# Performance work log

Hardware: AMD Instinct MI355X
Metric: run time of the kernel (lower is better)

The kernel has to match this reference:

```python
import jax, jax.numpy as jnp
import numpy as np

NUM_TOKENS = 50265  # roberta-base vocab size
CONTEXT_LEN = 384
BS = 4
N_DATASET = 2048


def setup_inputs() -> dict:
    key = jax.random.key(0)
    k1, k2, k3 = jax.random.split(key, 3)
    dataset_tokens = jax.random.randint(k1, (N_DATASET, CONTEXT_LEN), 0, NUM_TOKENS)
    input_tokens = jax.random.randint(k2, (BS, CONTEXT_LEN), 0, NUM_TOKENS)
    # t in (0,1): avoid exact endpoints where log((1-t)/T) -> -inf
    t = jax.random.uniform(k3, (BS,), minval=0.05, maxval=0.95, dtype=jnp.float32)
    return {"input_tokens": input_tokens, "dataset_tokens": dataset_tokens, "t": t}


def reference(input_tokens, dataset_tokens, t):
    """EmpiricalDFM.calculate_uniform_probabilities, dataset given as one array.

    flow[b,c,s] = sum_n exp(logp[n,b]) * onehot(dataset_tokens)[n,c,s] / sum_n exp(logp[n,b])
               = sum_n softmax_n(logp[:,b]) * onehot(dataset_tokens)[n,c,s]
    The original torch code computes exactly this via an online (streamed)
    log-sum-exp accumulation over dataset batches; softmax over the full
    dataset axis is the mathematically identical single-pass form.
    """
    bs, c = input_tokens.shape
    n = dataset_tokens.shape[0]
    T = NUM_TOKENS

    # (n, bs): number of positions where dataset row matches input row
    match_count = (dataset_tokens[:, None, :] == input_tokens[None, :, :]).sum(-1).astype(t.dtype)

    log_a = jnp.log(t + (1.0 - t) / T)          # (bs,) prob of match per position
    log_b = jnp.log((1.0 - t) / T)              # (bs,) prob of mismatch per position
    logp = match_count * log_a[None, :] + (c - match_count) * log_b[None, :]  # (n, bs)

    # Normalized weights over the dataset axis (stable log-sum-exp built in).
    w = jax.nn.softmax(logp, axis=0)            # (n, bs)

    # Weighted one-hot accumulate WITHOUT materializing the (n,c,V) one-hot:
    # flow[b, pos, dataset_tokens[j, pos]] += w[j, b]
    c_idx = jnp.broadcast_to(jnp.arange(c)[None, :], (n, c))
    flow = jnp.zeros((bs, c, T), dtype=t.dtype)
    flow = flow.at[:, c_idx, dataset_tokens].add(w.T[:, :, None])  # scatter over (bs, n, c)
    return flow
```

## Files before the change

kernel.cpp:

```cpp
#include <hip/hip_runtime.h>

constexpr int T_VOCAB = 50265;
constexpr int CLEN    = 384;
constexpr int BSZ     = 4;
constexpr int NDATA   = 2048;
constexpr int NPT     = NDATA / 256;
constexpr int CHUNK   = 12672;

template <bool WRITE_T>
__global__ __launch_bounds__(256) void k_match_logp(
    const int* __restrict__ in_tok,
    const int* __restrict__ ds_tok,
    const float* __restrict__ t,
    float* __restrict__ logp,
    int* __restrict__ dsT)
{
    __shared__ int s_in[BSZ * CLEN];
    __shared__ float s_la[BSZ], s_lb[BSZ];
    const int tid = threadIdx.x;
    for (int i = tid; i < BSZ * CLEN; i += 256) s_in[i] = in_tok[i];
    if (tid < BSZ) {
        float tv = t[tid];
        s_la[tid] = logf(tv + (1.0f - tv) / (float)T_VOCAB);
        s_lb[tid] = logf((1.0f - tv) / (float)T_VOCAB);
    }
    __syncthreads();

    const int n = blockIdx.x * 256 + tid;
    int mc0 = 0, mc1 = 0, mc2 = 0, mc3 = 0;
    const int4* row = (const int4*)(ds_tok + (size_t)n * CLEN);
    #pragma unroll 8
    for (int j = 0; j < CLEN / 4; ++j) {
        int4 v = row[j];
        int s = 4 * j;
        if (WRITE_T) {
            dsT[(size_t)(s + 0) * NDATA + n] = v.x;
            dsT[(size_t)(s + 1) * NDATA + n] = v.y;
            dsT[(size_t)(s + 2) * NDATA + n] = v.z;
            dsT[(size_t)(s + 3) * NDATA + n] = v.w;
        }
        mc0 += (v.x == s_in[0*CLEN+s]) + (v.y == s_in[0*CLEN+s+1]) + (v.z == s_in[0*CLEN+s+2]) + (v.w == s_in[0*CLEN+s+3]);
        mc1 += (v.x == s_in[1*CLEN+s]) + (v.y == s_in[1*CLEN+s+1]) + (v.z == s_in[1*CLEN+s+2]) + (v.w == s_in[1*CLEN+s+3]);
        mc2 += (v.x == s_in[2*CLEN+s]) + (v.y == s_in[2*CLEN+s+1]) + (v.z == s_in[2*CLEN+s+2]) + (v.w == s_in[2*CLEN+s+3]);
        mc3 += (v.x == s_in[3*CLEN+s]) + (v.y == s_in[3*CLEN+s+1]) + (v.z == s_in[3*CLEN+s+2]) + (v.w == s_in[3*CLEN+s+3]);
    }
    float m;
    m = (float)mc0; logp[0 * NDATA + n] = m * s_la[0] + ((float)CLEN - m) * s_lb[0];
    m = (float)mc1; logp[1 * NDATA + n] = m * s_la[1] + ((float)CLEN - m) * s_lb[1];
    m = (float)mc2; logp[2 * NDATA + n] = m * s_la[2] + ((float)CLEN - m) * s_lb[2];
    m = (float)mc3; logp[3 * NDATA + n] = m * s_la[3] + ((float)CLEN - m) * s_lb[3];
}

__global__ __launch_bounds__(256) void k_softmax(
    const float* __restrict__ logp,
    float* __restrict__ w)
{
    const int b = blockIdx.x;
    const int tid = threadIdx.x;
    float lp[NPT];
    float m = -INFINITY;
    #pragma unroll
    for (int k = 0; k < NPT; ++k) {
        lp[k] = logp[b * NDATA + tid + k * 256];
        m = fmaxf(m, lp[k]);
    }
    #pragma unroll
    for (int off = 32; off >= 1; off >>= 1) m = fmaxf(m, __shfl_xor(m, off));
    __shared__ float redm[4];
    __shared__ float reds[4];
    const int wid = tid >> 6;
    if ((tid & 63) == 0) redm[wid] = m;
    __syncthreads();
    const float M = fmaxf(fmaxf(redm[0], redm[1]), fmaxf(redm[2], redm[3]));

    float e[NPT];
    float sum = 0.0f;
    #pragma unroll
    for (int k = 0; k < NPT; ++k) { e[k] = expf(lp[k] - M); sum += e[k]; }
    #pragma unroll
    for (int off = 32; off >= 1; off >>= 1) sum += __shfl_xor(sum, off);
    if ((tid & 63) == 0) reds[wid] = sum;
    __syncthreads();
    const float inv = 1.0f / (reds[0] + reds[1] + reds[2] + reds[3]);
    #pragma unroll
    for (int k = 0; k < NPT; ++k) w[b * NDATA + tid + k * 256] = e[k] * inv;
}

template <bool USE_T>
__global__ __launch_bounds__(256) void k_scatter(
    const int* __restrict__ ds_tok,
    const int* __restrict__ dsT,
    const float* __restrict__ w,
    float* __restrict__ out)
{
    __shared__ float lds[CHUNK];
    const int tid = threadIdx.x;
    const int bid = blockIdx.x;
    const int b = bid & (BSZ - 1);
    const int s = bid >> 2;

    int   tok[NPT];
    float wv[NPT];
    #pragma unroll
    for (int k = 0; k < NPT; ++k) {
        const int n = tid + k * 256;
        tok[k] = USE_T ? dsT[(size_t)s * NDATA + n]
                       : ds_tok[(size_t)n * CLEN + s];
        wv[k] = w[b * NDATA + n];
    }

    float* rowp = out + ((size_t)b * CLEN + s) * T_VOCAB;
    const size_t row_elem0 = ((size_t)b * CLEN + s) * (size_t)T_VOCAB;

    for (int c0 = 0; c0 < T_VOCAB; c0 += CHUNK) {
        const int nch = (T_VOCAB - c0 < CHUNK) ? (T_VOCAB - c0) : CHUNK;
        for (int i = tid; i < nch; i += 256) lds[i] = 0.0f;
        __syncthreads();
        #pragma unroll
        for (int k = 0; k < NPT; ++k) {
            const unsigned off = (unsigned)(tok[k] - c0);
            if (off < (unsigned)nch) atomicAdd(&lds[off], wv[k]);
        }
        __syncthreads();
        const unsigned g0mod = (unsigned)((row_elem0 + (size_t)c0) & 3u);
        int head = (int)((4u - g0mod) & 3u);
        if (head > nch) head = nch;
        if (tid < head) rowp[c0 + tid] = lds[tid];
        const int rem = nch - head;
        const int nv = rem >> 2;
        float4* dst4 = (float4*)(rowp + c0 + head);
        for (int i = tid; i < nv; i += 256) {
            const int j = head + 4 * i;
            float4 v = { lds[j], lds[j + 1], lds[j + 2], lds[j + 3] };
            dst4[i] = v;
        }
        const int ts = head + (nv << 2);
        for (int i = ts + tid; i < nch; i += 256) rowp[c0 + i] = lds[i];
        __syncthreads();
    }
}

extern "C" void kernel_launch(void* const* d_in, const int* in_sizes, int n_in,
                              void* d_out, int out_size, void* d_ws, size_t ws_size,
                              hipStream_t stream) {
    const int*   in_tok = (const int*)d_in[0];
    const int*   ds_tok = (const int*)d_in[1];
    const float* t      = (const float*)d_in[2];
    float* out = (float*)d_out;

    float* logp = (float*)d_ws;
    float* w    = logp + (size_t)BSZ * NDATA;
    int*   dsT  = (int*)(w + (size_t)BSZ * NDATA);

    const size_t need = (size_t)2 * BSZ * NDATA * sizeof(float)
                      + (size_t)CLEN * NDATA * sizeof(int);
    const bool use_t = ws_size >= need;

    if (use_t) {
        k_match_logp<true><<<NDATA / 256, 256, 0, stream>>>(in_tok, ds_tok, t, logp, dsT);
    } else {
        k_match_logp<false><<<NDATA / 256, 256, 0, stream>>>(in_tok, ds_tok, t, logp, dsT);
    }
    k_softmax<<<BSZ, 256, 0, stream>>>(logp, w);
    if (use_t) {
        k_scatter<true><<<BSZ * CLEN, 256, 0, stream>>>(ds_tok, dsT, w, out);
    } else {
        k_scatter<false><<<BSZ * CLEN, 256, 0, stream>>>(ds_tok, dsT, w, out);
    }
}
```

Measured before the change: 351.9 us.

## Split match into tiled transpose plus sliced counting; fuse weights; nontemporal scatter stores

Replaces the single 8-block match kernel, which also wrote an uncoalesced transpose, with a shared-memory tiled transpose kernel and a 64-block sliced match-count kernel writing partial counts. A new weights kernel sums the partial counts, computes logp and does the softmax. The scatter kernel gets a smaller LDS chunk so more blocks fit per CU, an aligned LDS offset so it can copy whole vectors, and nontemporal vector stores for the large output. This adds two kernel launches and a partial-count buffer in exchange for more parallelism in the early stages and cheaper output writes.

```diff
diff --git a/kernel.cpp b/kernel.cpp
--- a/kernel.cpp
+++ b/kernel.cpp
@@ -5,69 +5,85 @@
 constexpr int BSZ     = 4;
 constexpr int NDATA   = 2048;
 constexpr int NPT     = NDATA / 256;
-constexpr int CHUNK   = 12672;
-
-template <bool WRITE_T>
-__global__ __launch_bounds__(256) void k_match_logp(
+constexpr int CHUNK   = 6720;
+constexpr int SLICES  = 8;
+constexpr int SCOLS   = CLEN / SLICES;
+
+typedef float f32x4 __attribute__((ext_vector_type(4)));
+
+__global__ __launch_bounds__(256) void k_transpose(
+    const int* __restrict__ ds, int* __restrict__ dsT)
+{
+    __shared__ int tile[64][65];
+    const int n0 = blockIdx.x * 64;
+    const int s0 = blockIdx.y * 64;
+    const int lane = threadIdx.x & 63;
+    const int quad = threadIdx.x >> 6;
+    #pragma unroll
+    for (int k = 0; k < 16; ++k) {
+        const int r = quad + 4 * k;
+        tile[r][lane] = ds[(size_t)(n0 + r) * CLEN + s0 + lane];
+    }
+    __syncthreads();
+    #pragma unroll
+    for (int k = 0; k < 16; ++k) {
+        const int c = quad + 4 * k;
+        dsT[(size_t)(s0 + c) * NDATA + n0 + lane] = tile[lane][c];
+    }
+}
+
+__global__ __launch_bounds__(256) void k_match(
+    const int* __restrict__ dsT,
     const int* __restrict__ in_tok,
-    const int* __restrict__ ds_tok,
+    int* __restrict__ pcount)
+{
+    const int nt = blockIdx.x & 7;
+    const int sl = blockIdx.x >> 3;
+    const int n  = nt * 256 + threadIdx.x;
+    const int sbase = sl * SCOLS;
+    int c0 = 0, c1 = 0, c2 = 0, c3 = 0;
+    #pragma unroll 4
+    for (int j = 0; j < SCOLS; ++j) {
+        const int s = sbase + j;
+        const int tok = dsT[(size_t)s * NDATA + n];
+        c0 += (tok == in_tok[0 * CLEN + s]);
+        c1 += (tok == in_tok[1 * CLEN + s]);
+        c2 += (tok == in_tok[2 * CLEN + s]);
+        c3 += (tok == in_tok[3 * CLEN + s]);
+    }
+    pcount[(sl * BSZ + 0) * NDATA + n] = c0;
+    pcount[(sl * BSZ + 1) * NDATA + n] = c1;
+    pcount[(sl * BSZ + 2) * NDATA + n] = c2;
+    pcount[(sl * BSZ + 3) * NDATA + n] = c3;
+}
+
+__global__ __launch_bounds__(256) void k_weights(
+    const int* __restrict__ pcount,
     const float* __restrict__ t,
-    float* __restrict__ logp,
-    int* __restrict__ dsT)
-{
-    __shared__ int s_in[BSZ * CLEN];
-    __shared__ float s_la[BSZ], s_lb[BSZ];
-    const int tid = threadIdx.x;
-    for (int i = tid; i < BSZ * CLEN; i += 256) s_in[i] = in_tok[i];
-    if (tid < BSZ) {
-        float tv = t[tid];
-        s_la[tid] = logf(tv + (1.0f - tv) / (float)T_VOCAB);
-        s_lb[tid] = logf((1.0f - tv) / (float)T_VOCAB);
-    }
-    __syncthreads();
-
-    const int n = blockIdx.x * 256 + tid;
-    int mc0 = 0, mc1 = 0, mc2 = 0, mc3 = 0;
-    const int4* row = (const int4*)(ds_tok + (size_t)n * CLEN);
-    #pragma unroll 8
-    for (int j = 0; j < CLEN / 4; ++j) {
-        int4 v = row[j];
-        int s = 4 * j;
-        if (WRITE_T) {
-            dsT[(size_t)(s + 0) * NDATA + n] = v.x;
-            dsT[(size_t)(s + 1) * NDATA + n] = v.y;
-            dsT[(size_t)(s + 2) * NDATA + n] = v.z;
-            dsT[(size_t)(s + 3) * NDATA + n] = v.w;
-        }
-        mc0 += (v.x == s_in[0*CLEN+s]) + (v.y == s_in[0*CLEN+s+1]) + (v.z == s_in[0*CLEN+s+2]) + (v.w == s_in[0*CLEN+s+3]);
-        mc1 += (v.x == s_in[1*CLEN+s]) + (v.y == s_in[1*CLEN+s+1]) + (v.z == s_in[1*CLEN+s+2]) + (v.w == s_in[1*CLEN+s+3]);
-        mc2 += (v.x == s_in[2*CLEN+s]) + (v.y == s_in[2*CLEN+s+1]) + (v.z == s_in[2*CLEN+s+2]) + (v.w == s_in[2*CLEN+s+3]);
-        mc3 += (v.x == s_in[3*CLEN+s]) + (v.y == s_in[3*CLEN+s+1]) + (v.z == s_in[3*CLEN+s+2]) + (v.w == s_in[3*CLEN+s+3]);
-    }
-    float m;
-    m = (float)mc0; logp[0 * NDATA + n] = m * s_la[0] + ((float)CLEN - m) * s_lb[0];
-    m = (float)mc1; logp[1 * NDATA + n] = m * s_la[1] + ((float)CLEN - m) * s_lb[1];
-    m = (float)mc2; logp[2 * NDATA + n] = m * s_la[2] + ((float)CLEN - m) * s_lb[2];
-    m = (float)mc3; logp[3 * NDATA + n] = m * s_la[3] + ((float)CLEN - m) * s_lb[3];
-}
-
-__global__ __launch_bounds__(256) void k_softmax(
-    const float* __restrict__ logp,
     float* __restrict__ w)
 {
     const int b = blockIdx.x;
     const int tid = threadIdx.x;
+    const float tv = t[b];
+    const float la = logf(tv + (1.0f - tv) / (float)T_VOCAB);
+    const float lb = logf((1.0f - tv) / (float)T_VOCAB);
+
     float lp[NPT];
     float m = -INFINITY;
     #pragma unroll
     for (int k = 0; k < NPT; ++k) {
-        lp[k] = logp[b * NDATA + tid + k * 256];
+        const int n = tid + k * 256;
+        int cnt = 0;
+        #pragma unroll
+        for (int sl = 0; sl < SLICES; ++sl)
+            cnt += pcount[(sl * BSZ + b) * NDATA + n];
+        const float mc = (float)cnt;
+        lp[k] = mc * la + ((float)CLEN - mc) * lb;
         m = fmaxf(m, lp[k]);
     }
     #pragma unroll
     for (int off = 32; off >= 1; off >>= 1) m = fmaxf(m, __shfl_xor(m, off));
-    __shared__ float redm[4];
-    __shared__ float reds[4];
+    __shared__ float redm[4], reds[4];
     const int wid = tid >> 6;
     if ((tid & 63) == 0) redm[wid] = m;
     __syncthreads();
@@ -93,7 +109,7 @@
     const float* __restrict__ w,
     float* __restrict__ out)
 {
-    __shared__ float lds[CHUNK];
+    __shared__ float lds[CHUNK + 4];
     const int tid = threadIdx.x;
     const int bid = blockIdx.x;
     const int b = bid & (BSZ - 1);
@@ -109,35 +125,99 @@
         wv[k] = w[b * NDATA + n];
     }
 
-    float* rowp = out + ((size_t)b * CLEN + s) * T_VOCAB;
     const size_t row_elem0 = ((size_t)b * CLEN + s) * (size_t)T_VOCAB;
+    float* rowp = out + row_elem0;
+    const int align_off = (int)(row_elem0 & 3);
 
     for (int c0 = 0; c0 < T_VOCAB; c0 += CHUNK) {
         const int nch = (T_VOCAB - c0 < CHUNK) ? (T_VOCAB - c0) : CHUNK;
-        for (int i = tid; i < nch; i += 256) lds[i] = 0.0f;
+        const int tot = nch + align_off;
+        f32x4* l4 = (f32x4*)lds;
+        const int nz4 = (tot + 3) >> 2;
+        for (int i = tid; i < nz4; i += 256) l4[i] = (f32x4){0.f, 0.f, 0.f, 0.f};
         __syncthreads();
         #pragma unroll
         for (int k = 0; k < NPT; ++k) {
             const unsigned off = (unsigned)(tok[k] - c0);
-            if (off < (unsigned)nch) atomicAdd(&lds[off], wv[k]);
+            if (off < (unsigned)nch) atomicAdd(&lds[off + align_off], wv[k]);
         }
         __syncthreads();
-        const unsigned g0mod = (unsigned)((row_elem0 + (size_t)c0) & 3u);
-        int head = (int)((4u - g0mod) & 3u);
+        int head = (4 - align_off) & 3;
         if (head > nch) head = nch;
-        if (tid < head) rowp[c0 + tid] = lds[tid];
-        const int rem = nch - head;
-        const int nv = rem >> 2;
-        float4* dst4 = (float4*)(rowp + c0 + head);
-        for (int i = tid; i < nv; i += 256) {
-            const int j = head + 4 * i;
-            float4 v = { lds[j], lds[j + 1], lds[j + 2], lds[j + 3] };
-            dst4[i] = v;
-        }
+        if (tid < head) rowp[c0 + tid] = lds[tid + align_off];
+        const int nv = (nch - head) >> 2;
+        const f32x4* l4s = (const f32x4*)lds + (align_off ? 1 : 0);
+        f32x4* dst4 = (f32x4*)(rowp + c0 + head);
+        for (int i = tid; i < nv; i += 256)
+            __builtin_nontemporal_store(l4s[i], &dst4[i]);
         const int ts = head + (nv << 2);
-        for (int i = ts + tid; i < nch; i += 256) rowp[c0 + i] = lds[i];
+        for (int i = ts + tid; i < nch; i += 256) rowp[c0 + i] = lds[i + align_off];
         __syncthreads();
     }
+}
+
+__global__ __launch_bounds__(256) void k_match_logp_fb(
+    const int* __restrict__ in_tok, const int* __restrict__ ds_tok,
+    const float* __restrict__ t, float* __restrict__ logp)
+{
+    __shared__ int s_in[BSZ * CLEN];
+    __shared__ float s_la[BSZ], s_lb[BSZ];
+    const int tid = threadIdx.x;
+    for (int i = tid; i < BSZ * CLEN; i += 256) s_in[i] = in_tok[i];
+    if (tid < BSZ) {
+        float tv = t[tid];
+        s_la[tid] = logf(tv + (1.0f - tv) / (float)T_VOCAB);
+        s_lb[tid] = logf((1.0f - tv) / (float)T_VOCAB);
+    }
+    __syncthreads();
+    const int n = blockIdx.x * 256 + tid;
+    int mc[BSZ] = {0, 0, 0, 0};
+    const int4* row = (const int4*)(ds_tok + (size_t)n * CLEN);
+    for (int j = 0; j < CLEN / 4; ++j) {
+        int4 v = row[j];
+        int s = 4 * j;
+        #pragma unroll
+        for (int b = 0; b < BSZ; ++b)
+            mc[b] += (v.x == s_in[b*CLEN+s]) + (v.y == s_in[b*CLEN+s+1]) +
+                     (v.z == s_in[b*CLEN+s+2]) + (v.w == s_in[b*CLEN+s+3]);
+    }
+    #pragma unroll
+    for (int b = 0; b < BSZ; ++b) {
+        float m = (float)mc[b];
+        logp[b * NDATA + n] = m * s_la[b] + ((float)CLEN - m) * s_lb[b];
+    }
+}
+
+__global__ __launch_bounds__(256) void k_softmax_fb(
+    const float* __restrict__ logp, float* __restrict__ w)
+{
+    const int b = blockIdx.x;
+    const int tid = threadIdx.x;
+    float lp[NPT];
+    float m = -INFINITY;
+    #pragma unroll
+    for (int k = 0; k < NPT; ++k) {
+        lp[k] = logp[b * NDATA + tid + k * 256];
+        m = fmaxf(m, lp[k]);
+    }
+    #pragma unroll
+    for (int off = 32; off >= 1; off >>= 1) m = fmaxf(m, __shfl_xor(m, off));
+    __shared__ float redm[4], reds[4];
+    const int wid = tid >> 6;
+    if ((tid & 63) == 0) redm[wid] = m;
+    __syncthreads();
+    const float M = fmaxf(fmaxf(redm[0], redm[1]), fmaxf(redm[2], redm[3]));
+    float e[NPT];
+    float sum = 0.0f;
+    #pragma unroll
+    for (int k = 0; k < NPT; ++k) { e[k] = expf(lp[k] - M); sum += e[k]; }
+    #pragma unroll
+    for (int off = 32; off >= 1; off >>= 1) sum += __shfl_xor(sum, off);
+    if ((tid & 63) == 0) reds[wid] = sum;
+    __syncthreads();
+    const float inv = 1.0f / (reds[0] + reds[1] + reds[2] + reds[3]);
+    #pragma unroll
+    for (int k = 0; k < NPT; ++k) w[b * NDATA + tid + k * 256] = e[k] * inv;
 }
 
 extern "C" void kernel_launch(void* const* d_in, const int* in_sizes, int n_in,
@@ -148,23 +228,22 @@
     const float* t      = (const float*)d_in[2];
     float* out = (float*)d_out;
 
-    float* logp = (float*)d_ws;
-    float* w    = logp + (size_t)BSZ * NDATA;
-    int*   dsT  = (int*)(w + (size_t)BSZ * NDATA);
-
-    const size_t need = (size_t)2 * BSZ * NDATA * sizeof(float)
-                      + (size_t)CLEN * NDATA * sizeof(int);
-    const bool use_t = ws_size >= need;
-
-    if (use_t) {
-        k_match_logp<true><<<NDATA / 256, 256, 0, stream>>>(in_tok, ds_tok, t, logp, dsT);
-    } else {
-        k_match_logp<false><<<NDATA / 256, 256, 0, stream>>>(in_tok, ds_tok, t, logp, dsT);
-    }
-    k_softmax<<<BSZ, 256, 0, stream>>>(logp, w);
-    if (use_t) {
+    int*   dsT    = (int*)d_ws;
+    int*   pcount = dsT + (size_t)CLEN * NDATA;
+    float* w      = (float*)(pcount + SLICES * BSZ * NDATA);
+    float* logp   = w + BSZ * NDATA;
+
+    const size_t need = ((size_t)CLEN * NDATA + (size_t)SLICES * BSZ * NDATA) * sizeof(int)
+                      + (size_t)2 * BSZ * NDATA * sizeof(float);
+
+    if (ws_size >= need) {
+        k_transpose<<<dim3(NDATA / 64, CLEN / 64), 256, 0, stream>>>(ds_tok, dsT);
+        k_match<<<64, 256, 0, stream>>>(dsT, in_tok, pcount);
+        k_weights<<<BSZ, 256, 0, stream>>>(pcount, t, w);
         k_scatter<true><<<BSZ * CLEN, 256, 0, stream>>>(ds_tok, dsT, w, out);
     } else {
+        k_match_logp_fb<<<NDATA / 256, 256, 0, stream>>>(in_tok, ds_tok, t, logp);
+        k_softmax_fb<<<BSZ, 256, 0, stream>>>(logp, w);
         k_scatter<false><<<BSZ * CLEN, 256, 0, stream>>>(ds_tok, dsT, w, out);
     }
 }
```

Result: faster. 344.4 us (-2.1%).
